# Kernel optimization log

Hardware: AMD Instinct MI355X
Metric: run time of the kernel (lower is better)

Reference implementation:

```python
import jax, jax.numpy as jnp
import numpy as np

NHEAD = 16
HEAD_DIM = 64
ROPE_BASE = 10000.0


def _rotate_half(x):
    # interleaved convention: pairs (x0,x1)->(-x1,x0)
    x1 = x[..., ::2]
    x2 = x[..., 1::2]
    return jnp.stack([-x2, x1], axis=-1).reshape(x.shape)


def _rope_cache(seq_len, head_dim, base):
    half = head_dim // 2
    inv_freq = 1.0 / base ** (jnp.arange(half, dtype=jnp.float32) / float(half))
    t = jnp.arange(seq_len, dtype=jnp.float32)
    freqs = jnp.einsum('i,j->ij', t, inv_freq)          # [T, half]
    emb = jnp.concatenate([freqs, freqs], axis=-1)      # [T, D] (half-half cat, matches torch source)
    return jnp.cos(emb), jnp.sin(emb)


def setup_inputs() -> dict:
    key = jax.random.key(0)
    k1, k2, k3 = jax.random.split(key, 3)
    b, t, c = 2, 2048, 1024
    x = jax.random.normal(k1, (b, t, c), dtype=jnp.float32)
    # torch nn.Linear weights: [out_features, in_features], scaled like kaiming-uniform-ish
    W_qkv = jax.random.normal(k2, (3 * c, c), dtype=jnp.float32) / np.sqrt(c)
    W_out = jax.random.normal(k3, (c, c), dtype=jnp.float32) / np.sqrt(c)
    return {"x": x, "W_qkv": W_qkv, "W_out": W_out}


def reference(x, W_qkv, W_out):
    b, t, c = x.shape
    nh, hd = NHEAD, HEAD_DIM
    qkv = x @ W_qkv.T                                   # [b, t, 3c]
    q, k, v = jnp.split(qkv, 3, axis=-1)

    def to_heads(a):
        return a.reshape(b, t, nh, hd).transpose(0, 2, 1, 3)  # [b, nh, t, hd]

    q, k, v = to_heads(q), to_heads(k), to_heads(v)
    cos, sin = _rope_cache(t, hd, ROPE_BASE)            # [t, hd]
    cos = cos.astype(q.dtype)[None, None]
    sin = sin.astype(q.dtype)[None, None]
    q = q * cos + _rotate_half(q) * sin
    k = k * cos + _rotate_half(k) * sin

    scale = 1.0 / np.sqrt(hd).astype(np.float32)
    scores = jnp.einsum('bhqd,bhkd->bhqk', q, k) * scale
    attn = jax.nn.softmax(scores, axis=-1)
    y = jnp.einsum('bhqk,bhkd->bhqd', attn, v)          # [b, nh, t, hd]
    y = y.transpose(0, 2, 1, 3).reshape(b, t, c)
    return y @ W_out.T
```

## Files before the change

### kernel.cpp

```cpp
#include <hip/hip_runtime.h>
#include <hip/hip_bf16.h>
#include <math.h>

typedef __hip_bfloat16 bf16;
typedef _Float16 f16;
typedef __attribute__((ext_vector_type(8))) short bf16x8;
typedef __attribute__((ext_vector_type(8))) _Float16 f16x8;
typedef __attribute__((ext_vector_type(4))) float f32x4;
typedef __attribute__((ext_vector_type(4))) unsigned u32x4;

#define MFMA_BF(a,b,c) __builtin_amdgcn_mfma_f32_16x16x32_bf16((a),(b),(c),0,0,0)
#define MFMA_F16(a,b,c) __builtin_amdgcn_mfma_f32_16x16x32_f16((a),(b),(c),0,0,0)

__device__ __forceinline__ void load_lds16(const void* g, void* l) {
  __builtin_amdgcn_global_load_lds(
      (__attribute__((address_space(1))) void*)(g),
      (__attribute__((address_space(3))) void*)(l), 16, 0, 0);
}

__device__ __forceinline__ unsigned pk_bf16(float a, float b) {
  unsigned ua = __builtin_bit_cast(unsigned, a);
  unsigned ub = __builtin_bit_cast(unsigned, b);
  ua += 0x7fffu + ((ua >> 16) & 1u);
  ub += 0x7fffu + ((ub >> 16) & 1u);
  return (ua >> 16) | (ub & 0xffff0000u);
}

__global__ void cvt_all(const float* __restrict__ x, const float* __restrict__ wq,
                        const float* __restrict__ wo, unsigned* __restrict__ xb,
                        unsigned* __restrict__ wqb, unsigned* __restrict__ wob) {
  int i = blockIdx.x * blockDim.x + threadIdx.x;
  const float* src;
  unsigned* dst;
  int off;
  if (i < 1048576) { src = x; dst = xb; off = i; }
  else if (i < 1048576 + 786432) { src = wq; dst = wqb; off = i - 1048576; }
  else { src = wo; dst = wob; off = i - (1048576 + 786432); }
  float4 v = reinterpret_cast<const float4*>(src)[off];
  uint2 u;
  u.x = pk_bf16(v.x, v.y);
  u.y = pk_bf16(v.z, v.w);
  reinterpret_cast<uint2*>(dst)[off] = u;
}

__global__ __launch_bounds__(256, 2)
void gemm_qkv(const bf16* __restrict__ A, const bf16* __restrict__ B,
              bf16* __restrict__ outq, bf16* __restrict__ outk,
              f16* __restrict__ outv) {
  __shared__ __align__(16) bf16 As[3][128 * 32];
  __shared__ __align__(16) bf16 Bs[3][128 * 32];
  const int K = 1024;
  const int tid = threadIdx.x;
  const int w = tid >> 6;
  const int lane = tid & 63;
  const int quad = lane >> 4;
  const int col = lane & 15;
  const int waveM = w >> 1;
  const int waveN = w & 1;
  const int bm = blockIdx.y * 128;
  const int bn = blockIdx.x * 128;

  f32x4 acc[4][4] = {};
  const int srow = lane >> 2;
  const int skoff = (((lane & 3) ^ ((srow >> 1) & 3))) * 8;
  const int swq = (quad ^ ((col >> 1) & 3)) * 8;

  auto stage = [&](int k0, int sb) {
#pragma unroll
    for (int p = 0; p < 2; ++p) {
      int r = p * 64 + w * 16 + srow;
      load_lds16(A + (size_t)(bm + r) * K + k0 + skoff,
                 (char*)As + sb * 8192 + p * 4096 + w * 1024);
      load_lds16(B + (size_t)(bn + r) * K + k0 + skoff,
                 (char*)Bs + sb * 8192 + p * 4096 + w * 1024);
    }
  };

  stage(0, 0);
  stage(32, 1);

  int cb = 0;
  for (int k0 = 0; k0 < K; k0 += 32) {
    if (k0 + 32 < K) __asm__ volatile("s_waitcnt vmcnt(4)" ::: "memory");
    else             __asm__ volatile("s_waitcnt vmcnt(0)" ::: "memory");
    __asm__ volatile("s_barrier" ::: "memory");
    if (k0 + 64 < K) {
      int nb = cb + 2; if (nb >= 3) nb -= 3;
      stage(k0 + 64, nb);
    }
    const bf16* at = &As[cb][0];
    const bf16* bt = &Bs[cb][0];
    bf16x8 af[4], bfr[4];
#pragma unroll
    for (int i = 0; i < 4; ++i)
      af[i] = *reinterpret_cast<const bf16x8*>(at + (waveM * 64 + i * 16 + col) * 32 + swq);
#pragma unroll
    for (int j = 0; j < 4; ++j)
      bfr[j] = *reinterpret_cast<const bf16x8*>(bt + (waveN * 64 + j * 16 + col) * 32 + swq);
#pragma unroll
    for (int i = 0; i < 4; ++i)
#pragma unroll
      for (int j = 0; j < 4; ++j)
        acc[i][j] = MFMA_BF(af[i], bfr[j], acc[i][j]);
    cb = (cb == 2) ? 0 : cb + 1;
  }

  if (bn < 2048) {
    const float NEGK = -0.4152410118f;
    const float C1 = 0.1803368799f;
    const float sgn = (col & 1) ? 1.0f : -1.0f;
#pragma unroll
    for (int j = 0; j < 4; ++j) {
      const int n0 = bn + waveN * 64 + j * 16;
      const int sel = n0 >> 10;
      const int hh = (n0 & 1023) >> 6;
      const int dd = (n0 & 63) + col;
      bf16* outp = sel ? outk : outq;
      const float post = sel ? 1.0f : C1;
      const float invf = __builtin_amdgcn_exp2f((float)((n0 & 31) + col) * NEGK);
#pragma unroll
      for (int i = 0; i < 4; ++i) {
#pragma unroll
        for (int r = 0; r < 4; ++r) {
          int m = bm + waveM * 64 + i * 16 + quad * 4 + r;
          int b = m >> 11, t = m & 2047;
          float v = acc[i][j][r];
          float partner = __shfl_xor(v, 1);
          float ang = (float)t * invf;
          float res = (v * __cosf(ang) + sgn * partner * __sinf(ang)) * post;
          outp[((size_t)(b * 16 + hh) * 2048 + t) * 64 + dd] = __float2bfloat16(res);
        }
      }
    }
  } else {
    const int b = bm >> 11;
    const int tt0 = (bm & 2047) + waveM * 64;
#pragma unroll
    for (int j = 0; j < 4; ++j) {
      const int n0 = bn + waveN * 64 + j * 16;
      const int hh = (n0 & 1023) >> 6;
      const int dd = (n0 & 63) + col;
      f16* dst = outv + (size_t)(b * 16 + hh) * 131072 + (size_t)dd * 2048;
#pragma unroll
      for (int i = 0; i < 4; ++i) {
        uint2 pk;
        pk.x = __builtin_bit_cast(unsigned, __builtin_amdgcn_cvt_pkrtz(acc[i][j][0], acc[i][j][1]));
        pk.y = __builtin_bit_cast(unsigned, __builtin_amdgcn_cvt_pkrtz(acc[i][j][2], acc[i][j][3]));
        *reinterpret_cast<uint2*>(dst + tt0 + i * 16 + quad * 4) = pk;
      }
    }
  }
}

__global__ __launch_bounds__(256, 2)
void gemm_out(const bf16* __restrict__ A, const bf16* __restrict__ B,
              float* __restrict__ outf) {
  __shared__ __align__(16) bf16 As[3][64 * 32];
  __shared__ __align__(16) bf16 Bs[3][128 * 32];
  const int K = 1024;
  const int tid = threadIdx.x;
  const int w = tid >> 6;
  const int lane = tid & 63;
  const int quad = lane >> 4;
  const int col = lane & 15;
  const int bm = blockIdx.y * 64;
  const int bn = blockIdx.x * 128;

  f32x4 acc[4][2] = {};
  const int srow = lane >> 2;
  const int skoff = (((lane & 3) ^ ((srow >> 1) & 3))) * 8;
  const int swq = (quad ^ ((col >> 1) & 3)) * 8;

  auto stage = [&](int k0, int sb) {
    load_lds16(A + (size_t)(bm + w * 16 + srow) * K + k0 + skoff,
               (char*)As + sb * 4096 + w * 1024);
#pragma unroll
    for (int p = 0; p < 2; ++p)
      load_lds16(B + (size_t)(bn + p * 64 + w * 16 + srow) * K + k0 + skoff,
                 (char*)Bs + sb * 8192 + p * 4096 + w * 1024);
  };

  stage(0, 0);
  stage(32, 1);

  int cb = 0;
  for (int k0 = 0; k0 < K; k0 += 32) {
    if (k0 + 32 < K) __asm__ volatile("s_waitcnt vmcnt(3)" ::: "memory");
    else             __asm__ volatile("s_waitcnt vmcnt(0)" ::: "memory");
    __asm__ volatile("s_barrier" ::: "memory");
    if (k0 + 64 < K) {
      int nb = cb + 2; if (nb >= 3) nb -= 3;
      stage(k0 + 64, nb);
    }
    const bf16* at = &As[cb][0];
    const bf16* bt = &Bs[cb][0];
    bf16x8 af[4], bfr[2];
#pragma unroll
    for (int i = 0; i < 4; ++i)
      af[i] = *reinterpret_cast<const bf16x8*>(at + (i * 16 + col) * 32 + swq);
#pragma unroll
    for (int j = 0; j < 2; ++j)
      bfr[j] = *reinterpret_cast<const bf16x8*>(bt + (w * 32 + j * 16 + col) * 32 + swq);
#pragma unroll
    for (int i = 0; i < 4; ++i)
#pragma unroll
      for (int j = 0; j < 2; ++j)
        acc[i][j] = MFMA_BF(af[i], bfr[j], acc[i][j]);
    cb = (cb == 2) ? 0 : cb + 1;
  }

#pragma unroll
  for (int i = 0; i < 4; ++i)
#pragma unroll
    for (int j = 0; j < 2; ++j) {
      const int n0 = bn + w * 32 + j * 16;
#pragma unroll
      for (int r = 0; r < 4; ++r) {
        int m = bm + i * 16 + quad * 4 + r;
        outf[(size_t)m * 1024 + n0 + col] = acc[i][j][r];
      }
    }
}

__global__ __launch_bounds__(256, 3)
void attn_kernel(const bf16* __restrict__ qh, const bf16* __restrict__ kh,
                 const f16* __restrict__ vt, bf16* __restrict__ y) {
  __shared__ __align__(16) bf16 Ks[3][64 * 64];
  __shared__ __align__(16) f16 Vs[3][64 * 64];

  const int bh = blockIdx.y;
  const int w = threadIdx.x >> 6;
  const int lane = threadIdx.x & 63;
  const int quad = lane >> 4;
  const int col = lane & 15;

  const int qrow0 = blockIdx.x * 128 + w * 32 + col;
  bf16x8 qf[2][2];
#pragma unroll
  for (int f = 0; f < 2; ++f)
#pragma unroll
    for (int c = 0; c < 2; ++c)
      qf[f][c] = *reinterpret_cast<const bf16x8*>(
          qh + ((size_t)bh * 2048 + qrow0 + f * 16) * 64 + c * 32 + quad * 8);

  const int s8 = lane >> 3;
  const int blk = (lane & 7) ^ s8;
  const bf16* kg = kh + (size_t)bh * 2048 * 64;
  const f16* vg = vt + (size_t)bh * 64 * 2048;
  const int ks0 = 32 * (w >> 1) + 8 * ((4 * w + (s8 >> 2)) & 3) + 4 * (w & 1) + (s8 & 3);
  const int ks1 = 32 * (w >> 1) + 8 * ((4 * w + 2 + (s8 >> 2)) & 3) + 4 * (w & 1) + (s8 & 3);
  const int vrow0 = w * 16 + s8;

  const int csw = col & 7;
  const int sw0 = (quad ^ csw) * 8;
  const int sw1 = ((quad + 4) ^ csw) * 8;
  const int rdbase = col * 64;

  f32x4 O[2][4] = {};
  float l[2] = {};

  auto stage = [&](int kn, int sb) {
    char* kb = (char*)Ks + sb * 8192 + w * 2048;
    char* vb = (char*)Vs + sb * 8192 + w * 2048;
    load_lds16(kg + (size_t)(kn + ks0) * 64 + blk * 8, kb);
    load_lds16(kg + (size_t)(kn + ks1) * 64 + blk * 8, kb + 1024);
    load_lds16(vg + (size_t)vrow0 * 2048 + kn + blk * 8, vb);
    load_lds16(vg + (size_t)(vrow0 + 8) * 2048 + kn + blk * 8, vb + 1024);
  };

  stage(0, 0);
  stage(64, 1);

  int cb = 0;
  for (int kc = 0; kc < 2048; kc += 64) {
    if (kc + 64 < 2048) __asm__ volatile("s_waitcnt vmcnt(4)" ::: "memory");
    else                __asm__ volatile("s_waitcnt vmcnt(0)" ::: "memory");
    __asm__ volatile("s_barrier" ::: "memory");
    if (kc + 128 < 2048) {
      int nb = cb + 2; if (nb >= 3) nb -= 3;
      stage(kc + 128, nb);
    }

    const bf16* kt = &Ks[cb][0];
    const f16* vtile = &Vs[cb][0];

    f32x4 s[2][4];
#pragma unroll
    for (int t = 0; t < 4; ++t) {
      bf16x8 kf0 = *reinterpret_cast<const bf16x8*>(kt + t * 1024 + rdbase + sw0);
      bf16x8 kf1 = *reinterpret_cast<const bf16x8*>(kt + t * 1024 + rdbase + sw1);
#pragma unroll
      for (int f = 0; f < 2; ++f) {
        f32x4 a = {};
        a = MFMA_BF(kf0, qf[f][0], a);
        a = MFMA_BF(kf1, qf[f][1], a);
        s[f][t] = a;
      }
    }

    f16x8 pf[2][2];
#pragma unroll
    for (int f = 0; f < 2; ++f) {
      unsigned pk[8];
      float lf = 0.0f;
#pragma unroll
      for (int t = 0; t < 4; ++t) {
        float p0 = __builtin_amdgcn_exp2f(s[f][t][0]);
        float p1 = __builtin_amdgcn_exp2f(s[f][t][1]);
        float p2 = __builtin_amdgcn_exp2f(s[f][t][2]);
        float p3 = __builtin_amdgcn_exp2f(s[f][t][3]);
        lf += (p0 + p1) + (p2 + p3);
        pk[t * 2]     = __builtin_bit_cast(unsigned, __builtin_amdgcn_cvt_pkrtz(p0, p1));
        pk[t * 2 + 1] = __builtin_bit_cast(unsigned, __builtin_amdgcn_cvt_pkrtz(p2, p3));
      }
      l[f] += lf;
      pf[f][0] = __builtin_bit_cast(f16x8, (u32x4){pk[0], pk[1], pk[2], pk[3]});
      pf[f][1] = __builtin_bit_cast(f16x8, (u32x4){pk[4], pk[5], pk[6], pk[7]});
    }

#pragma unroll
    for (int j = 0; j < 4; ++j) {
      f16x8 vf0 = *reinterpret_cast<const f16x8*>(vtile + j * 1024 + rdbase + sw0);
      f16x8 vf1 = *reinterpret_cast<const f16x8*>(vtile + j * 1024 + rdbase + sw1);
#pragma unroll
      for (int f = 0; f < 2; ++f) {
        O[f][j] = MFMA_F16(vf0, pf[f][0], O[f][j]);
        O[f][j] = MFMA_F16(vf1, pf[f][1], O[f][j]);
      }
    }
    cb = (cb == 2) ? 0 : cb + 1;
  }

  const int b = bh >> 4, h = bh & 15;
#pragma unroll
  for (int f = 0; f < 2; ++f) {
    float lv = l[f];
    lv += __shfl_xor(lv, 16, 64);
    lv += __shfl_xor(lv, 32, 64);
    float inv = 1.0f / lv;
    int tq = blockIdx.x * 128 + w * 32 + f * 16 + col;
    size_t base = ((size_t)b * 2048 + tq) * 1024 + h * 64;
#pragma unroll
    for (int j = 0; j < 4; ++j) {
      uint2 pk2;
      pk2.x = pk_bf16(O[f][j][0] * inv, O[f][j][1] * inv);
      pk2.y = pk_bf16(O[f][j][2] * inv, O[f][j][3] * inv);
      *reinterpret_cast<uint2*>((unsigned short*)y + base + j * 16 + quad * 4) = pk2;
    }
  }
}

extern "C" void kernel_launch(void* const* d_in, const int* in_sizes, int n_in,
                              void* d_out, int out_size, void* d_ws, size_t ws_size,
                              hipStream_t stream) {
  const float* x    = (const float*)d_in[0];
  const float* wqkv = (const float*)d_in[1];
  const float* wout = (const float*)d_in[2];
  float* out = (float*)d_out;
  char* ws = (char*)d_ws;

  bf16* xb    = (bf16*)(ws);
  bf16* wqkvb = (bf16*)(ws + (size_t)(8 << 20));
  bf16* woutb = (bf16*)(ws + (size_t)(14 << 20));
  bf16* qh    = (bf16*)(ws + (size_t)(16 << 20));
  bf16* kh    = (bf16*)(ws + (size_t)(24 << 20));
  f16*  vt    = (f16*) (ws + (size_t)(32 << 20));
  bf16* y     = (bf16*)(ws + (size_t)(40 << 20));

  cvt_all<<<8192, 256, 0, stream>>>(x, wqkv, wout,
                                    (unsigned*)xb, (unsigned*)wqkvb, (unsigned*)woutb);
  gemm_qkv<<<dim3(24, 32), 256, 0, stream>>>(xb, wqkvb, qh, kh, vt);
  attn_kernel<<<dim3(16, 32), 256, 0, stream>>>(qh, kh, vt, y);
  gemm_out<<<dim3(8, 64), 256, 0, stream>>>(y, woutb, out);
}
```

Baseline: 177.2 us.

## Split attention over two KV halves and merge partial outputs in a new kernel

Attention is split along the key dimension into two halves (grid z=2), so twice as many blocks run. Each half writes unnormalized fp16 partial outputs and row sums, and a new merge kernel adds them and normalizes into bf16 y. The pipeline also goes from triple to double buffering with an extra barrier before the V reads, which cuts LDS and allows occupancy 4. The cost is an extra launch plus partial-output memory traffic. Because the kernel skips max subtraction, the two halves can be summed directly, but holding unnormalized sums in fp16 risks overflow or precision loss.

```diff
diff --git a/kernel.cpp b/kernel.cpp
--- a/kernel.cpp
+++ b/kernel.cpp
@@ -222,13 +222,16 @@
     }
 }
 
-__global__ __launch_bounds__(256, 3)
+__global__ __launch_bounds__(256, 4)
 void attn_kernel(const bf16* __restrict__ qh, const bf16* __restrict__ kh,
-                 const f16* __restrict__ vt, bf16* __restrict__ y) {
-  __shared__ __align__(16) bf16 Ks[3][64 * 64];
-  __shared__ __align__(16) f16 Vs[3][64 * 64];
+                 const f16* __restrict__ vt, f16* __restrict__ Op0,
+                 f16* __restrict__ Op1, float* __restrict__ lp) {
+  __shared__ __align__(16) bf16 Ks[2][64 * 64];
+  __shared__ __align__(16) f16 Vs[2][64 * 64];
 
   const int bh = blockIdx.y;
+  const int sp = blockIdx.z;
+  const int kc0 = sp << 10;
   const int w = threadIdx.x >> 6;
   const int lane = threadIdx.x & 63;
   const int quad = lane >> 4;
@@ -268,18 +271,14 @@
     load_lds16(vg + (size_t)(vrow0 + 8) * 2048 + kn + blk * 8, vb + 1024);
   };
 
-  stage(0, 0);
-  stage(64, 1);
+  stage(kc0, 0);
 
   int cb = 0;
-  for (int kc = 0; kc < 2048; kc += 64) {
-    if (kc + 64 < 2048) __asm__ volatile("s_waitcnt vmcnt(4)" ::: "memory");
-    else                __asm__ volatile("s_waitcnt vmcnt(0)" ::: "memory");
+  for (int kc = kc0; kc < kc0 + 1024; kc += 64) {
+    const bool more = (kc + 64 < kc0 + 1024);
+    __asm__ volatile("s_waitcnt vmcnt(2)" ::: "memory");
     __asm__ volatile("s_barrier" ::: "memory");
-    if (kc + 128 < 2048) {
-      int nb = cb + 2; if (nb >= 3) nb -= 3;
-      stage(kc + 128, nb);
-    }
+    if (more) stage(kc + 64, cb ^ 1);
 
     const bf16* kt = &Ks[cb][0];
     const f16* vtile = &Vs[cb][0];
@@ -318,6 +317,10 @@
       pf[f][1] = __builtin_bit_cast(f16x8, (u32x4){pk[4], pk[5], pk[6], pk[7]});
     }
 
+    if (more) __asm__ volatile("s_waitcnt vmcnt(4)" ::: "memory");
+    else      __asm__ volatile("s_waitcnt vmcnt(0)" ::: "memory");
+    __asm__ volatile("s_barrier" ::: "memory");
+
 #pragma unroll
     for (int j = 0; j < 4; ++j) {
       f16x8 vf0 = *reinterpret_cast<const f16x8*>(vtile + j * 1024 + rdbase + sw0);
@@ -328,26 +331,51 @@
         O[f][j] = MFMA_F16(vf1, pf[f][1], O[f][j]);
       }
     }
-    cb = (cb == 2) ? 0 : cb + 1;
-  }
-
-  const int b = bh >> 4, h = bh & 15;
+    cb ^= 1;
+  }
+
+  f16* op = sp ? Op1 : Op0;
 #pragma unroll
   for (int f = 0; f < 2; ++f) {
     float lv = l[f];
     lv += __shfl_xor(lv, 16, 64);
     lv += __shfl_xor(lv, 32, 64);
-    float inv = 1.0f / lv;
     int tq = blockIdx.x * 128 + w * 32 + f * 16 + col;
-    size_t base = ((size_t)b * 2048 + tq) * 1024 + h * 64;
+    size_t row = (size_t)bh * 2048 + tq;
+    if (quad == 0) lp[(size_t)sp * 65536 + row] = lv;
+    f16* dst = op + row * 64;
 #pragma unroll
     for (int j = 0; j < 4; ++j) {
       uint2 pk2;
-      pk2.x = pk_bf16(O[f][j][0] * inv, O[f][j][1] * inv);
-      pk2.y = pk_bf16(O[f][j][2] * inv, O[f][j][3] * inv);
-      *reinterpret_cast<uint2*>((unsigned short*)y + base + j * 16 + quad * 4) = pk2;
-    }
-  }
+      pk2.x = __builtin_bit_cast(unsigned, __builtin_amdgcn_cvt_pkrtz(O[f][j][0], O[f][j][1]));
+      pk2.y = __builtin_bit_cast(unsigned, __builtin_amdgcn_cvt_pkrtz(O[f][j][2], O[f][j][3]));
+      *reinterpret_cast<uint2*>(dst + j * 16 + quad * 4) = pk2;
+    }
+  }
+}
+
+__global__ void attn_merge(const f16* __restrict__ Op0, const f16* __restrict__ Op1,
+                           const float* __restrict__ lp, bf16* __restrict__ y) {
+  int i = blockIdx.x * blockDim.x + threadIdx.x;
+  int d8 = i & 7;
+  int t  = (i >> 3) & 2047;
+  int bh = i >> 14;
+  size_t row = (size_t)bh * 2048 + t;
+  float inv = 1.0f / (lp[row] + lp[row + 65536]);
+  size_t o = row * 64 + d8 * 8;
+  f16x8 a = *reinterpret_cast<const f16x8*>(Op0 + o);
+  f16x8 b = *reinterpret_cast<const f16x8*>(Op1 + o);
+  int bb = bh >> 4, h = bh & 15;
+  unsigned short* dst =
+      (unsigned short*)y + ((size_t)(bb * 2048 + t) * 1024 + h * 64 + d8 * 8);
+  u32x4 r;
+#pragma unroll
+  for (int k = 0; k < 4; ++k) {
+    float v0 = ((float)a[2 * k]     + (float)b[2 * k])     * inv;
+    float v1 = ((float)a[2 * k + 1] + (float)b[2 * k + 1]) * inv;
+    r[k] = pk_bf16(v0, v1);
+  }
+  *reinterpret_cast<u32x4*>(dst) = r;
 }
 
 extern "C" void kernel_launch(void* const* d_in, const int* in_sizes, int n_in,
@@ -366,10 +394,14 @@
   bf16* kh    = (bf16*)(ws + (size_t)(24 << 20));
   f16*  vt    = (f16*) (ws + (size_t)(32 << 20));
   bf16* y     = (bf16*)(ws + (size_t)(40 << 20));
+  f16*  op0   = (f16*) (ws);
+  f16*  op1   = (f16*) (ws + (size_t)(48 << 20));
+  float* lpart= (float*)(ws + (size_t)(56 << 20));
 
   cvt_all<<<8192, 256, 0, stream>>>(x, wqkv, wout,
                                     (unsigned*)xb, (unsigned*)wqkvb, (unsigned*)woutb);
   gemm_qkv<<<dim3(24, 32), 256, 0, stream>>>(xb, wqkvb, qh, kh, vt);
-  attn_kernel<<<dim3(16, 32), 256, 0, stream>>>(qh, kh, vt, y);
+  attn_kernel<<<dim3(16, 32, 2), 256, 0, stream>>>(qh, kh, vt, op0, op1, lpart);
+  attn_merge<<<2048, 256, 0, stream>>>(op0, op1, lpart, y);
   gemm_out<<<dim3(8, 64), 256, 0, stream>>>(y, woutb, out);
 }
```

New measurement: 188.2 us. 1.06x slower.

## Software-pipeline QK^T of next tile with PV of previous tile in attention

Applied to the files above, without the earlier changes.

Restructures the attention loop so that each iteration computes the QK^T scores for the current K tile while issuing the PV MFMAs for the previous tile's probabilities. Softmax of the current tile then runs after the matrix work, so exp/convert work can overlap with other waves' MFMAs. Adds s_setprio around the MFMA blocks, a prologue and epilogue, a 2-deep K buffer with a 3-deep V buffer, and lowers the launch-bounds occupancy hint from 3 to 2. The extra live state (pf held across iterations) raises register pressure and may reduce occupancy.

```diff
diff --git a/kernel.cpp b/kernel.cpp
--- a/kernel.cpp
+++ b/kernel.cpp
@@ -222,10 +222,10 @@
     }
 }
 
-__global__ __launch_bounds__(256, 3)
+__global__ __launch_bounds__(256, 2)
 void attn_kernel(const bf16* __restrict__ qh, const bf16* __restrict__ kh,
                  const f16* __restrict__ vt, bf16* __restrict__ y) {
-  __shared__ __align__(16) bf16 Ks[3][64 * 64];
+  __shared__ __align__(16) bf16 Ks[2][64 * 64];
   __shared__ __align__(16) f16 Vs[3][64 * 64];
 
   const int bh = blockIdx.y;
@@ -258,47 +258,20 @@
 
   f32x4 O[2][4] = {};
   float l[2] = {};
-
-  auto stage = [&](int kn, int sb) {
-    char* kb = (char*)Ks + sb * 8192 + w * 2048;
-    char* vb = (char*)Vs + sb * 8192 + w * 2048;
-    load_lds16(kg + (size_t)(kn + ks0) * 64 + blk * 8, kb);
-    load_lds16(kg + (size_t)(kn + ks1) * 64 + blk * 8, kb + 1024);
-    load_lds16(vg + (size_t)vrow0 * 2048 + kn + blk * 8, vb);
-    load_lds16(vg + (size_t)(vrow0 + 8) * 2048 + kn + blk * 8, vb + 1024);
+  f16x8 pf[2][2];
+
+  auto stageK = [&](int kn, int kb) {
+    char* kbp = (char*)Ks + kb * 8192 + w * 2048;
+    load_lds16(kg + (size_t)(kn + ks0) * 64 + blk * 8, kbp);
+    load_lds16(kg + (size_t)(kn + ks1) * 64 + blk * 8, kbp + 1024);
   };
-
-  stage(0, 0);
-  stage(64, 1);
-
-  int cb = 0;
-  for (int kc = 0; kc < 2048; kc += 64) {
-    if (kc + 64 < 2048) __asm__ volatile("s_waitcnt vmcnt(4)" ::: "memory");
-    else                __asm__ volatile("s_waitcnt vmcnt(0)" ::: "memory");
-    __asm__ volatile("s_barrier" ::: "memory");
-    if (kc + 128 < 2048) {
-      int nb = cb + 2; if (nb >= 3) nb -= 3;
-      stage(kc + 128, nb);
-    }
-
-    const bf16* kt = &Ks[cb][0];
-    const f16* vtile = &Vs[cb][0];
-
-    f32x4 s[2][4];
-#pragma unroll
-    for (int t = 0; t < 4; ++t) {
-      bf16x8 kf0 = *reinterpret_cast<const bf16x8*>(kt + t * 1024 + rdbase + sw0);
-      bf16x8 kf1 = *reinterpret_cast<const bf16x8*>(kt + t * 1024 + rdbase + sw1);
-#pragma unroll
-      for (int f = 0; f < 2; ++f) {
-        f32x4 a = {};
-        a = MFMA_BF(kf0, qf[f][0], a);
-        a = MFMA_BF(kf1, qf[f][1], a);
-        s[f][t] = a;
-      }
-    }
-
-    f16x8 pf[2][2];
+  auto stageV = [&](int kn, int vb) {
+    char* vbp = (char*)Vs + vb * 8192 + w * 2048;
+    load_lds16(vg + (size_t)vrow0 * 2048 + kn + blk * 8, vbp);
+    load_lds16(vg + (size_t)(vrow0 + 8) * 2048 + kn + blk * 8, vbp + 1024);
+  };
+
+  auto softmax = [&](f32x4 (&s)[2][4]) {
 #pragma unroll
     for (int f = 0; f < 2; ++f) {
       unsigned pk[8];
@@ -317,18 +290,91 @@
       pf[f][0] = __builtin_bit_cast(f16x8, (u32x4){pk[0], pk[1], pk[2], pk[3]});
       pf[f][1] = __builtin_bit_cast(f16x8, (u32x4){pk[4], pk[5], pk[6], pk[7]});
     }
-
-#pragma unroll
-    for (int j = 0; j < 4; ++j) {
-      f16x8 vf0 = *reinterpret_cast<const f16x8*>(vtile + j * 1024 + rdbase + sw0);
-      f16x8 vf1 = *reinterpret_cast<const f16x8*>(vtile + j * 1024 + rdbase + sw1);
+  };
+
+  stageK(0, 0);
+  stageV(0, 0);
+
+  __asm__ volatile("s_waitcnt vmcnt(2)" ::: "memory");
+  __asm__ volatile("s_barrier" ::: "memory");
+  stageK(64, 1);
+  stageV(64, 1);
+  {
+    const bf16* kt = &Ks[0][0];
+    f32x4 s[2][4];
+    __builtin_amdgcn_s_setprio(1);
+#pragma unroll
+    for (int t = 0; t < 4; ++t) {
+      bf16x8 kf0 = *reinterpret_cast<const bf16x8*>(kt + t * 1024 + rdbase + sw0);
+      bf16x8 kf1 = *reinterpret_cast<const bf16x8*>(kt + t * 1024 + rdbase + sw1);
 #pragma unroll
       for (int f = 0; f < 2; ++f) {
-        O[f][j] = MFMA_F16(vf0, pf[f][0], O[f][j]);
-        O[f][j] = MFMA_F16(vf1, pf[f][1], O[f][j]);
-      }
-    }
-    cb = (cb == 2) ? 0 : cb + 1;
+        f32x4 a = {};
+        a = MFMA_BF(kf0, qf[f][0], a);
+        a = MFMA_BF(kf1, qf[f][1], a);
+        s[f][t] = a;
+      }
+    }
+    __builtin_amdgcn_s_setprio(0);
+    softmax(s);
+  }
+
+  int vprev = 0;
+  int vnext = 2;
+#pragma unroll 1
+  for (int c = 1; c < 32; ++c) {
+    const int kc = c * 64;
+    __asm__ volatile("s_waitcnt vmcnt(2)" ::: "memory");
+    __asm__ volatile("s_barrier" ::: "memory");
+    if (c + 1 < 32) {
+      stageK(kc + 64, (c + 1) & 1);
+      stageV(kc + 64, vnext);
+    }
+
+    const bf16* kt = &Ks[c & 1][0];
+    const f16* vtile = &Vs[vprev][0];
+
+    f32x4 s[2][4];
+    __builtin_amdgcn_s_setprio(1);
+#pragma unroll
+    for (int t = 0; t < 4; ++t) {
+      bf16x8 kf0 = *reinterpret_cast<const bf16x8*>(kt + t * 1024 + rdbase + sw0);
+      bf16x8 kf1 = *reinterpret_cast<const bf16x8*>(kt + t * 1024 + rdbase + sw1);
+      f16x8 vf0 = *reinterpret_cast<const f16x8*>(vtile + t * 1024 + rdbase + sw0);
+      f16x8 vf1 = *reinterpret_cast<const f16x8*>(vtile + t * 1024 + rdbase + sw1);
+#pragma unroll
+      for (int f = 0; f < 2; ++f) {
+        f32x4 a = {};
+        a = MFMA_BF(kf0, qf[f][0], a);
+        a = MFMA_BF(kf1, qf[f][1], a);
+        s[f][t] = a;
+        O[f][t] = MFMA_F16(vf0, pf[f][0], O[f][t]);
+        O[f][t] = MFMA_F16(vf1, pf[f][1], O[f][t]);
+      }
+    }
+    __builtin_amdgcn_s_setprio(0);
+    softmax(s);
+
+    vprev = (vprev == 2) ? 0 : vprev + 1;
+    vnext = (vnext == 2) ? 0 : vnext + 1;
+  }
+
+  __asm__ volatile("s_waitcnt vmcnt(0)" ::: "memory");
+  __asm__ volatile("s_barrier" ::: "memory");
+  {
+    const f16* vtile = &Vs[vprev][0];
+    __builtin_amdgcn_s_setprio(1);
+#pragma unroll
+    for (int t = 0; t < 4; ++t) {
+      f16x8 vf0 = *reinterpret_cast<const f16x8*>(vtile + t * 1024 + rdbase + sw0);
+      f16x8 vf1 = *reinterpret_cast<const f16x8*>(vtile + t * 1024 + rdbase + sw1);
+#pragma unroll
+      for (int f = 0; f < 2; ++f) {
+        O[f][t] = MFMA_F16(vf0, pf[f][0], O[f][t]);
+        O[f][t] = MFMA_F16(vf1, pf[f][1], O[f][t]);
+      }
+    }
+    __builtin_amdgcn_s_setprio(0);
   }
 
   const int b = bh >> 4, h = bh & 15;
```

New measurement: 178.1 us. No clear change (+0.5%).
